# Kernel tuning notes

Hardware: AMD Instinct MI355X
Metric: run time of the kernel (lower is better)

Reference implementation:

```python
import jax, jax.numpy as jnp
import numpy as np

K, N, D, M, M_RF, N_RF = 512, 512, 16, 64, 16, 64


def cmul(a, b):
    # complex matmul with stacked real/imag in axis -3: a [...,2,m,k], b [...,2,k,n]
    ar, ai = a[..., 0, :, :], a[..., 1, :, :]
    br, bi = b[..., 0, :, :], b[..., 1, :, :]
    return jnp.stack([ar @ br - ai @ bi, ar @ bi + ai @ br], axis=-3)


def conjT(a):
    # complex conjugate transpose
    ar, ai = a[..., 0, :, :], a[..., 1, :, :]
    return jnp.stack([jnp.swapaxes(ar, -1, -2), -jnp.swapaxes(ai, -1, -2)], axis=-3)


def cinv(a):
    # inverse of complex matrix a=[2,n,n] via real 2n x 2n block matrix
    ar, ai = a[0], a[1]
    n = ar.shape[0]
    Mblk = jnp.block([[ar, -ai], [ai, ar]])
    Minv = jnp.linalg.inv(Mblk)
    return jnp.stack([Minv[:n, :n], Minv[n:, :n]], axis=0)


def setup_inputs() -> dict:
    key = jax.random.key(0)
    ks = jax.random.split(key, 8)
    s = 0.05  # keep accumulated products well-scaled
    H = s * jax.random.normal(ks[0], (K, 2, M, N), jnp.float32)
    U_RF = s * jax.random.normal(ks[1], (K, 2, M, M_RF), jnp.float32)
    U_BB = s * jax.random.normal(ks[2], (K, 2, M_RF, D), jnp.float32)
    W = s * jax.random.normal(ks[3], (K, 2, D, D), jnp.float32)
    V_RF = s * jax.random.normal(ks[4], (2, N, N_RF), jnp.float32)
    V_BB = s * jax.random.normal(ks[5], (K, 2, N_RF, D), jnp.float32)
    Y = s * jax.random.normal(ks[6], (K, 2, N, D), jnp.float32)
    rho = jnp.ones((1,), jnp.float32)  # forward arg, unused by the module
    rho_X_layer = jnp.asarray(6.0, jnp.float32)  # learned scalar
    mu = jnp.asarray(1.0, jnp.float32)           # learned scalar
    params4 = 0.001 * jax.random.normal(ks[7], (K, 2, N, D), jnp.float32)
    return dict(H=H, U_RF=U_RF, U_BB=U_BB, W=W, V_RF=V_RF, V_BB=V_BB, Y=Y,
                rho=rho, rho_X_layer=rho_X_layer, mu=mu, params4=params4)


def reference(H, U_RF, U_BB, W, V_RF, V_BB, Y, rho, rho_X_layer, mu, params4):
    # temp[k] = H[k]^H U_RF[k] U_BB[k] : [K,2,N,d]
    temp = cmul(cmul(conjT(H), U_RF), U_BB)
    TW = cmul(temp, W)  # [K,2,N,d]
    # A_rho = sum_k temp W temp^H + I/(2 rho) : [2,N,N]
    A_rho = cmul(TW, conjT(temp)).sum(axis=0)
    I = jnp.stack([jnp.eye(N, dtype=H.dtype), jnp.zeros((N, N), H.dtype)], axis=0)
    A_rho = A_rho + (1.0 / (2.0 * rho_X_layer)) * I
    # B_rho[k] = temp W + 0.5*(V_RF V_BB[k]/rho - Y[k]) : [K,2,N,d]
    B_rho = TW + 0.5 * ((1.0 / rho_X_layer) * cmul(V_RF, V_BB) - Y)
    A_inv = cinv(A_rho + mu * I)  # [2,N,N]
    X = cmul(A_inv, B_rho) + params4  # [K,2,N,d]
    return X
```

## Files before the change

### kernel.cpp

```cpp
#include <hip/hip_runtime.h>

#define KK 512
#define NN 512
#define DD 16
#define MM 64
#define MRF 16
#define NRF 64

typedef __attribute__((ext_vector_type(8))) short bf16x8;
typedef __attribute__((ext_vector_type(4))) float f32x4;
typedef __attribute__((ext_vector_type(8))) unsigned short u16x8;
typedef __attribute__((ext_vector_type(4))) unsigned short u16x4;

#define MFMA16 __builtin_amdgcn_mfma_f32_16x16x32_bf16

static __device__ __forceinline__ unsigned short f2bf(float x) {
    unsigned int u = __float_as_uint(x);
    u += 0x7fffu + ((u >> 16) & 1u);
    return (unsigned short)(u >> 16);
}
static __device__ __forceinline__ float bf2f(unsigned short b) {
    return __uint_as_float((unsigned int)b << 16);
}
static __device__ __forceinline__ unsigned int pk2(float lo, float hi) {
    return (unsigned int)f2bf(lo) | ((unsigned int)f2bf(hi) << 16);
}

union frag_cast { uint4 u; bf16x8 v; };

__global__ __launch_bounds__(256) void vrfb_kernel(
    const float* __restrict__ V_RF, unsigned short* __restrict__ VRFb)
{
    const int idx = blockIdx.x*256 + threadIdx.x;
    const int n = idx >> 7, j = idx & 127;
    const int p = j >> 6, r = j & 63;
    VRFb[idx] = f2bf(V_RF[((size_t)p*NN + n)*NRF + r]);
}

__global__ __launch_bounds__(256) void small_kernel(
    const float* __restrict__ U_RF, const float* __restrict__ U_BB,
    const float* __restrict__ W, const float* __restrict__ V_BB,
    unsigned int* __restrict__ GT2p, unsigned int* __restrict__ VBT2p)
{
    const int k = blockIdx.x, t = threadIdx.x;
    __shared__ float sUR[2][MM][17];
    __shared__ float sUB[2][MRF][DD], sW[2][DD][DD];
    __shared__ float sVB[2][NRF][17];
    __shared__ float sG[2][MM][17], sGW[2][MM][17];

    const float* uf = U_RF + (size_t)k*2*MM*MRF;
    for (int i = t; i < 2*MM*MRF; i += 256) sUR[i>>10][(i>>4)&63][i&15] = uf[i];
    const float* ub = U_BB + (size_t)k*2*MRF*DD;
    for (int i = t; i < 2*MRF*DD; i += 256) sUB[i>>8][(i>>4)&15][i&15] = ub[i];
    const float* ww = W + (size_t)k*2*DD*DD;
    for (int i = t; i < 2*DD*DD; i += 256) sW[i>>8][(i>>4)&15][i&15] = ww[i];
    const float* vb = V_BB + (size_t)k*2*NRF*DD;
    for (int i = t; i < 2*NRF*DD; i += 256) sVB[i>>10][(i>>4)&63][i&15] = vb[i];
    __syncthreads();

    {
        const int m = t >> 2, dq = (t & 3) * 4;
        float gr[4] = {0,0,0,0}, gi[4] = {0,0,0,0};
#pragma unroll
        for (int r = 0; r < MRF; ++r) {
            const float ur = sUR[0][m][r], ui = sUR[1][m][r];
#pragma unroll
            for (int q = 0; q < 4; ++q) {
                const float br = sUB[0][r][dq+q], bi = sUB[1][r][dq+q];
                gr[q] += ur*br - ui*bi;
                gi[q] += ur*bi + ui*br;
            }
        }
#pragma unroll
        for (int q = 0; q < 4; ++q) { sG[0][m][dq+q] = gr[q]; sG[1][m][dq+q] = gi[q]; }
    }
    __syncthreads();

    {
        const int m = t >> 2, dq = (t & 3) * 4;
        float gwr[4] = {0,0,0,0}, gwi[4] = {0,0,0,0};
#pragma unroll
        for (int dp = 0; dp < DD; ++dp) {
            const float gr = sG[0][m][dp], gi = sG[1][m][dp];
#pragma unroll
            for (int q = 0; q < 4; ++q) {
                const float wr = sW[0][dp][dq+q], wi = sW[1][dp][dq+q];
                gwr[q] += gr*wr - gi*wi;
                gwi[q] += gr*wi + gi*wr;
            }
        }
#pragma unroll
        for (int q = 0; q < 4; ++q) { sGW[0][m][dq+q] = gwr[q]; sGW[1][m][dq+q] = gwi[q]; }
    }
    __syncthreads();

    {
        const int e2 = t >> 2;
        const int col0 = (t & 3) * 16;
        const int m0 = (2*e2) & 63, hi0 = (2*e2) >> 6;
        const int m1 = (2*e2+1) & 63, hi1 = (2*e2+1) >> 6;
        unsigned int* dst = GT2p + ((size_t)k*64 + e2)*64 + col0;
#pragma unroll
        for (int jb = 0; jb < 4; ++jb) {
            uint4 o;
#pragma unroll
            for (int jj = 0; jj < 4; ++jj) {
                const int col = col0 + jb*4 + jj;
                const int s = col >> 4, d = col & 15;
                const float (*P)[MM][17] = (s < 2) ? sG : sGW;
                const int im = s & 1;
                float v0, v1;
                if (!im) { v0 = hi0 ? P[1][m0][d] : P[0][m0][d];
                           v1 = hi1 ? P[1][m1][d] : P[0][m1][d]; }
                else     { v0 = hi0 ? -P[0][m0][d] : P[1][m0][d];
                           v1 = hi1 ? -P[0][m1][d] : P[1][m1][d]; }
                ((unsigned int*)&o)[jj] = pk2(v0, v1);
            }
            *reinterpret_cast<uint4*>(dst + jb*4) = o;
        }
    }
    if (t < 128) {
        const int e2 = t >> 1;
        const int col0 = (t & 1) * 16;
        const int r0 = (2*e2) & 63, hi0 = (2*e2) >> 6;
        const int r1 = (2*e2+1) & 63, hi1 = (2*e2+1) >> 6;
        unsigned int* dst = VBT2p + ((size_t)k*64 + e2)*32 + col0;
#pragma unroll
        for (int jb = 0; jb < 4; ++jb) {
            uint4 o;
#pragma unroll
            for (int jj = 0; jj < 4; ++jj) {
                const int col = col0 + jb*4 + jj;
                const int s = col >> 4, d = col & 15;
                float v0, v1;
                if (s == 0) { v0 = hi0 ? -sVB[1][r0][d] : sVB[0][r0][d];
                              v1 = hi1 ? -sVB[1][r1][d] : sVB[0][r1][d]; }
                else        { v0 = hi0 ?  sVB[0][r0][d] : sVB[1][r0][d];
                              v1 = hi1 ?  sVB[0][r1][d] : sVB[1][r1][d]; }
                ((unsigned int*)&o)[jj] = pk2(v0, v1);
            }
            *reinterpret_cast<uint4*>(dst + jb*4) = o;
        }
    }
}

__global__ __launch_bounds__(512) void prep_main(
    const float* __restrict__ H, const unsigned int* __restrict__ GT2p,
    const unsigned int* __restrict__ VBT2p, const unsigned short* __restrict__ VRFb,
    const float* __restrict__ Y, const float* __restrict__ rhoX,
    unsigned short* __restrict__ tempb, unsigned short* __restrict__ TWb,
    unsigned short* __restrict__ Bb)
{
    const int nb = blockIdx.x & 3;
    const int k  = blockIdx.x >> 2;
    const int t  = threadIdx.x;
    const int n0 = nb*128;

    __shared__ unsigned int sH[64][129];
    __shared__ unsigned int sG[64][65];
    __shared__ unsigned int sV[64][33];

    const float* Hk = H + (size_t)k*128*NN + n0;
#pragma unroll
    for (int pass = 0; pass < 4; ++pass) {
        const int e2 = pass*16 + (t >> 5);
        const int c4 = (t & 31) * 4;
        const float4 a = *reinterpret_cast<const float4*>(Hk + (size_t)(2*e2  )*NN + c4);
        const float4 b = *reinterpret_cast<const float4*>(Hk + (size_t)(2*e2+1)*NN + c4);
        uint4 d;
        d.x = pk2(a.x, b.x); d.y = pk2(a.y, b.y);
        d.z = pk2(a.z, b.z); d.w = pk2(a.w, b.w);
        *reinterpret_cast<uint4*>(&sH[e2][c4]) = d;
    }
    {
        const unsigned int* g = GT2p + (size_t)k*4096;
        const int e2 = t >> 3, c0 = (t & 7) * 8;
        *reinterpret_cast<uint4*>(&sG[e2][c0])     = *reinterpret_cast<const uint4*>(g + e2*64 + c0);
        *reinterpret_cast<uint4*>(&sG[e2][c0 + 4]) = *reinterpret_cast<const uint4*>(g + e2*64 + c0 + 4);
    }
    if (t < 256) {
        const unsigned int* v = VBT2p + (size_t)k*2048;
        const int e2 = t >> 2, c0 = (t & 3) * 8;
        *reinterpret_cast<uint4*>(&sV[e2][c0])     = *reinterpret_cast<const uint4*>(v + e2*32 + c0);
        *reinterpret_cast<uint4*>(&sV[e2][c0 + 4]) = *reinterpret_cast<const uint4*>(v + e2*32 + c0 + 4);
    }
    __syncthreads();

    const int w = t >> 6, lane = t & 63;
    const int c = lane & 15, kg = lane >> 4;
    const float irx = 1.f / rhoX[0];
    const int ncol = w*16 + c;
    const int n = n0 + ncol;

    f32x4 aTr = (f32x4)0.f, aTi = (f32x4)0.f;
    f32x4 aWr = (f32x4)0.f, aWi = (f32x4)0.f;
    f32x4 aVr = (f32x4)0.f, aVi = (f32x4)0.f;

#pragma unroll
    for (int ks = 0; ks < 4; ++ks) {
        const int slot0 = ks*32 + kg*8;
        const int e2b = ks*16 + kg*4;
        frag_cast fh, g0, g1, g2, g3, v0, v1;
#pragma unroll
        for (int q = 0; q < 4; ++q) {
            ((unsigned int*)&fh.u)[q] = sH[e2b+q][ncol];
            ((unsigned int*)&g0.u)[q] = sG[e2b+q][c];
            ((unsigned int*)&g1.u)[q] = sG[e2b+q][16 + c];
            ((unsigned int*)&g2.u)[q] = sG[e2b+q][32 + c];
            ((unsigned int*)&g3.u)[q] = sG[e2b+q][48 + c];
            ((unsigned int*)&v0.u)[q] = sV[e2b+q][c];
            ((unsigned int*)&v1.u)[q] = sV[e2b+q][16 + c];
        }
        const bf16x8 bv = *reinterpret_cast<const bf16x8*>(VRFb + (size_t)n*128 + slot0);

        aTr = MFMA16(g0.v, fh.v, aTr, 0, 0, 0);
        aTi = MFMA16(g1.v, fh.v, aTi, 0, 0, 0);
        aWr = MFMA16(g2.v, fh.v, aWr, 0, 0, 0);
        aWi = MFMA16(g3.v, fh.v, aWi, 0, 0, 0);
        aVr = MFMA16(v0.v, bv, aVr, 0, 0, 0);
        aVi = MFMA16(v1.v, bv, aVi, 0, 0, 0);
    }

    {
        const size_t o0 = ((size_t)(k*2 + 0)*NN + n)*DD + kg*4;
        const size_t o1 = ((size_t)(k*2 + 1)*NN + n)*DD + kg*4;
        const float4 y0 = *reinterpret_cast<const float4*>(Y + o0);
        const float4 y1 = *reinterpret_cast<const float4*>(Y + o1);
        const float y0a[4] = {y0.x, y0.y, y0.z, y0.w};
        const float y1a[4] = {y1.x, y1.y, y1.z, y1.w};
        u16x4 tr_, ti_, wr_, wi_, br_, bi_;
#pragma unroll
        for (int r = 0; r < 4; ++r) {
            tr_[r] = f2bf(aTr[r]);  ti_[r] = f2bf(aTi[r]);
            wr_[r] = f2bf(aWr[r]);  wi_[r] = f2bf(aWi[r]);
            br_[r] = f2bf(aWr[r] + 0.5f*(aVr[r]*irx - y0a[r]));
            bi_[r] = f2bf(aWi[r] + 0.5f*(aVi[r]*irx - y1a[r]));
        }
        *reinterpret_cast<u16x4*>(tempb + o0) = tr_;
        *reinterpret_cast<u16x4*>(tempb + o1) = ti_;
        *reinterpret_cast<u16x4*>(TWb + o0)   = wr_;
        *reinterpret_cast<u16x4*>(TWb + o1)   = wi_;
        *reinterpret_cast<u16x4*>(Bb + o0)    = br_;
        *reinterpret_cast<u16x4*>(Bb + o1)    = bi_;
    }
}

__global__ __launch_bounds__(256) void egemm_kernel(
    const unsigned short* __restrict__ TWb, const unsigned short* __restrict__ tmpb,
    float* __restrict__ Epart)
{
    const int ib = blockIdx.x >> 3;
    const int ks = blockIdx.x & 7;
    const int jb = blockIdx.y;
    const int w    = threadIdx.x >> 6;
    const int lane = threadIdx.x & 63;
    const int m  = lane & 15;
    const int kg = lane >> 4;
    const int iw = ib*64 + (w>>1)*32;
    const int jw = jb*64 + (w&1)*32;
    const int d0  = (kg & 1) * 8;
    const int kof = kg >> 1;

    f32x4 RR[2][2], II[2][2], RI[2][2], IR[2][2];
#pragma unroll
    for (int is = 0; is < 2; ++is)
#pragma unroll
        for (int js = 0; js < 2; ++js) {
            RR[is][js] = (f32x4)0.f; II[is][js] = (f32x4)0.f;
            RI[is][js] = (f32x4)0.f; IR[is][js] = (f32x4)0.f;
        }

#pragma unroll 2
    for (int c = 0; c < 32; ++c) {
        const int chunk = ks*32 + c;
        const int kp = chunk*2 + kof;
        const unsigned short* Ab = TWb  + ((size_t)(kp*2+0)*NN + iw + m)*DD + d0;
        const unsigned short* Bb2 = tmpb + ((size_t)(kp*2+0)*NN + jw + m)*DD + d0;
        bf16x8 ar[2], ai[2], br[2], bi[2];
#pragma unroll
        for (int is = 0; is < 2; ++is) {
            ar[is] = *reinterpret_cast<const bf16x8*>(Ab + (size_t)is*16*DD);
            ai[is] = *reinterpret_cast<const bf16x8*>(Ab + (size_t)NN*DD + (size_t)is*16*DD);
        }
#pragma unroll
        for (int js = 0; js < 2; ++js) {
            br[js] = *reinterpret_cast<const bf16x8*>(Bb2 + (size_t)js*16*DD);
            bi[js] = *reinterpret_cast<const bf16x8*>(Bb2 + (size_t)NN*DD + (size_t)js*16*DD);
        }
#pragma unroll
        for (int is = 0; is < 2; ++is)
#pragma unroll
            for (int js = 0; js < 2; ++js) {
                RR[is][js] = MFMA16(ar[is], br[js], RR[is][js], 0, 0, 0);
                II[is][js] = MFMA16(ai[is], bi[js], II[is][js], 0, 0, 0);
                RI[is][js] = MFMA16(ar[is], bi[js], RI[is][js], 0, 0, 0);
                IR[is][js] = MFMA16(ai[is], br[js], IR[is][js], 0, 0, 0);
            }
    }

    float* Eb = Epart + (size_t)ks*2*NN*NN;
#pragma unroll
    for (int is = 0; is < 2; ++is)
#pragma unroll
        for (int js = 0; js < 2; ++js) {
            const int i = iw + is*16 + kg*4;
            const int jx = jw + js*16 + m;
#pragma unroll
            for (int r = 0; r < 4; ++r) {
                Eb[(size_t)(i+r)*NN + jx]               = RR[is][js][r] + II[is][js][r];
                Eb[(size_t)NN*NN + (size_t)(i+r)*NN + jx] = IR[is][js][r] - RI[is][js][r];
            }
        }
}

__global__ __launch_bounds__(256) void reduceinit_kernel(
    const float* __restrict__ Epart,
    const float* __restrict__ rhoX, const float* __restrict__ mu,
    unsigned short* __restrict__ P, unsigned short* __restrict__ PT,
    unsigned short* __restrict__ T1, unsigned short* __restrict__ T1T)
{
    const size_t idx = (size_t)blockIdx.x*256 + threadIdx.x;
    const float ic = 1.f / (1.f/(2.f*rhoX[0]) + mu[0]);
    const size_t pl = (size_t)2*NN*NN;
    float s = 0.f;
#pragma unroll
    for (int ks = 0; ks < 8; ++ks) s += Epart[(size_t)ks*pl + idx];
    const float mm = s * ic;
    const int p = (int)(idx / ((size_t)NN*NN));
    const size_t rem = idx - (size_t)p*NN*NN;
    const int i = (int)(rem / NN), jx = (int)(rem % NN);
    const unsigned short pv = f2bf(-mm);
    const unsigned short tv = f2bf(((p == 0 && i == jx) ? 1.f : 0.f) - mm);
    const size_t tidx = (size_t)p*NN*NN + (size_t)jx*NN + i;
    P[idx] = pv;  PT[tidx] = pv;
    T1[idx] = tv; T1T[tidx] = tv;
}

template<bool ADD_B, bool WRITE_T>
__global__ __launch_bounds__(256) void mm_kernel(
    const unsigned short* __restrict__ A, const unsigned short* __restrict__ BT,
    unsigned short* __restrict__ D, unsigned short* __restrict__ DT)
{
    const int w    = threadIdx.x >> 6;
    const int lane = threadIdx.x & 63;
    const int m  = lane & 15;
    const int kg = lane >> 4;
    const int i0 = blockIdx.y*32;
    const int j0 = blockIdx.x*32;
    const int iw = (w>>1)*16;
    const int jw = (w&1)*16;

    __shared__ unsigned short sD[2][32][34];

    f32x4 RR = (f32x4)0.f, II = (f32x4)0.f, RI = (f32x4)0.f, IR = (f32x4)0.f;

#pragma unroll 8
    for (int c = 0; c < 16; ++c) {
        const int l0 = c*32 + kg*8;
        const bf16x8 ar = *reinterpret_cast<const bf16x8*>(A  + (size_t)(i0+iw+m)*NN + l0);
        const bf16x8 ai = *reinterpret_cast<const bf16x8*>(A  + (size_t)NN*NN + (size_t)(i0+iw+m)*NN + l0);
        const bf16x8 br = *reinterpret_cast<const bf16x8*>(BT + (size_t)(j0+jw+m)*NN + l0);
        const bf16x8 bi = *reinterpret_cast<const bf16x8*>(BT + (size_t)NN*NN + (size_t)(j0+jw+m)*NN + l0);
        RR = MFMA16(ar, br, RR, 0, 0, 0);
        II = MFMA16(ai, bi, II, 0, 0, 0);
        RI = MFMA16(ar, bi, RI, 0, 0, 0);
        IR = MFMA16(ai, br, IR, 0, 0, 0);
    }
    const int i = i0 + iw + kg*4;
    const int jx = j0 + jw + m;
    float adr[4] = {0.f,0.f,0.f,0.f}, adi[4] = {0.f,0.f,0.f,0.f};
    if (ADD_B) {
        const u16x4 badr = *reinterpret_cast<const u16x4*>(BT + (size_t)jx*NN + i);
        const u16x4 badi = *reinterpret_cast<const u16x4*>(BT + (size_t)NN*NN + (size_t)jx*NN + i);
#pragma unroll
        for (int r = 0; r < 4; ++r) { adr[r] = bf2f(badr[r]); adi[r] = bf2f(badi[r]); }
    }
#pragma unroll
    for (int r = 0; r < 4; ++r) {
        const unsigned short dr_ = f2bf(RR[r] - II[r] + adr[r]);
        const unsigned short di_ = f2bf(RI[r] + IR[r] + adi[r]);
        D[(size_t)(i+r)*NN + jx] = dr_;
        D[(size_t)NN*NN + (size_t)(i+r)*NN + jx] = di_;
        if (WRITE_T) {
            sD[0][iw + kg*4 + r][jw + m] = dr_;
            sD[1][iw + kg*4 + r][jw + m] = di_;
        }
    }
    if (WRITE_T) {
        __syncthreads();
        const int t = threadIdx.x;
        const int r8 = t >> 2, seg = t & 3;
        const int plane = r8 >> 5, jloc = r8 & 31;
        u16x8 v;
#pragma unroll
        for (int e = 0; e < 8; ++e) v[e] = sD[plane][seg*8 + e][jloc];
        *reinterpret_cast<u16x8*>(DT + (size_t)plane*NN*NN +
                                  (size_t)(j0 + jloc)*NN + i0 + seg*8) = v;
    }
}

__global__ __launch_bounds__(256) void final_kernel(
    const unsigned short* __restrict__ Sb, const unsigned short* __restrict__ Bb,
    const float* __restrict__ par4,
    const float* __restrict__ rhoX, const float* __restrict__ mu,
    float* __restrict__ Xout)
{
    const int k0 = blockIdx.x * 2;
    __shared__ __align__(16) unsigned short sBT[2][2][DD][520];

#pragma unroll
    for (int kk = 0; kk < 2; ++kk) {
        const unsigned short* Bk = Bb + (size_t)(k0 + kk)*2*NN*DD;
        for (int q = 0; q < 8; ++q) {
            const int t8 = q*256 + threadIdx.x;
            const u16x8 v = *reinterpret_cast<const u16x8*>(Bk + (size_t)t8*8);
            const int flat = t8*8;
            const int p = flat >> 13, n = (flat >> 4) & 511, dd0 = flat & 15;
#pragma unroll
            for (int jj = 0; jj < 8; ++jj) sBT[kk][p][dd0+jj][n] = v[jj];
        }
    }
    __syncthreads();

    const int w    = threadIdx.x >> 6;
    const int lane = threadIdx.x & 63;
    const int m  = lane & 15;
    const int kg = lane >> 4;
    const int i0 = blockIdx.y*64 + w*16;

    f32x4 RR[2], II[2], RI[2], IR[2];
#pragma unroll
    for (int kk = 0; kk < 2; ++kk) {
        RR[kk] = (f32x4)0.f; II[kk] = (f32x4)0.f;
        RI[kk] = (f32x4)0.f; IR[kk] = (f32x4)0.f;
    }

#pragma unroll 2
    for (int c = 0; c < 16; ++c) {
        const int l0 = c*32 + kg*8;
        const bf16x8 ar = *reinterpret_cast<const bf16x8*>(Sb + (size_t)(i0+m)*NN + l0);
        const bf16x8 ai = *reinterpret_cast<const bf16x8*>(Sb + (size_t)NN*NN + (size_t)(i0+m)*NN + l0);
#pragma unroll
        for (int kk = 0; kk < 2; ++kk) {
            const bf16x8 br = *reinterpret_cast<const bf16x8*>(&sBT[kk][0][m][l0]);
            const bf16x8 bi = *reinterpret_cast<const bf16x8*>(&sBT[kk][1][m][l0]);
            RR[kk] = MFMA16(ar, br, RR[kk], 0, 0, 0);
            II[kk] = MFMA16(ai, bi, II[kk], 0, 0, 0);
            RI[kk] = MFMA16(ar, bi, RI[kk], 0, 0, 0);
            IR[kk] = MFMA16(ai, br, IR[kk], 0, 0, 0);
        }
    }
    const float ic = 1.f / (1.f/(2.f*rhoX[0]) + mu[0]);
#pragma unroll
    for (int kk = 0; kk < 2; ++kk) {
        const int k = k0 + kk;
#pragma unroll
        for (int r = 0; r < 4; ++r) {
            const int i = i0 + kg*4 + r;
            const int d = m;
            const size_t idx0 = ((size_t)(k*2+0)*NN + i)*DD + d;
            const size_t idx1 = ((size_t)(k*2+1)*NN + i)*DD + d;
            Xout[idx0] = (RR[kk][r] - II[kk][r])*ic + par4[idx0];
            Xout[idx1] = (RI[kk][r] + IR[kk][r])*ic + par4[idx1];
        }
    }
}

extern "C" void kernel_launch(void* const* d_in, const int* in_sizes, int n_in,
                              void* d_out, int out_size, void* d_ws, size_t ws_size,
                              hipStream_t stream) {
    const float* H     = (const float*)d_in[0];
    const float* U_RF  = (const float*)d_in[1];
    const float* U_BB  = (const float*)d_in[2];
    const float* W     = (const float*)d_in[3];
    const float* V_RF  = (const float*)d_in[4];
    const float* V_BB  = (const float*)d_in[5];
    const float* Y     = (const float*)d_in[6];
    const float* rhoX  = (const float*)d_in[8];
    const float* mu    = (const float*)d_in[9];
    const float* par4  = (const float*)d_in[10];
    float* Xout = (float*)d_out;

    unsigned short* u = (unsigned short*)d_ws;
    const size_t bigE = (size_t)KK*2*NN*DD;
    const size_t plE  = (size_t)2*NN*NN;
    unsigned short* tempb = u;
    unsigned short* TWb   = tempb + bigE;
    unsigned short* Bb    = TWb + bigE;
    unsigned int*   GT2p  = (unsigned int*)(Bb + bigE);
    unsigned int*   VBT2p = GT2p + (size_t)KK*4096;
    unsigned short* VRFb  = (unsigned short*)(VBT2p + (size_t)KK*2048);
    unsigned short* Pm    = VRFb + (size_t)NN*128;
    unsigned short* PmT   = Pm  + plE;
    unsigned short* T1    = PmT + plE;
    unsigned short* T1T   = T1  + plE;
    unsigned short* Q     = T1T + plE;
    unsigned short* QT    = Q   + plE;
    unsigned short* R     = QT  + plE;
    unsigned short* RT    = R   + plE;
    unsigned short* T2    = RT  + plE;
    unsigned short* T2T   = T2  + plE;
    unsigned short* T3    = T2T + plE;
    unsigned short* T3T   = T3  + plE;
    unsigned short* R2    = T3T + plE;
    unsigned short* Ss    = R2  + plE;
    float* Epart = (float*)(Ss + plE);

    vrfb_kernel<<<256, 256, 0, stream>>>(V_RF, VRFb);
    small_kernel<<<KK, 256, 0, stream>>>(U_RF, U_BB, W, V_BB, GT2p, VBT2p);
    prep_main<<<KK*4, 512, 0, stream>>>(H, GT2p, VBT2p, VRFb, Y, rhoX,
                                        tempb, TWb, Bb);
    egemm_kernel<<<dim3(64, 8), 256, 0, stream>>>(TWb, tempb, Epart);
    reduceinit_kernel<<<(int)(plE/256), 256, 0, stream>>>(Epart, rhoX, mu,
                                                          Pm, PmT, T1, T1T);
    mm_kernel<false,true ><<<dim3(16,16), 256, 0, stream>>>(Pm, PmT, Q,  QT);
    mm_kernel<true ,true ><<<dim3(16,16), 256, 0, stream>>>(Q,  T1T, T2, T2T);
    mm_kernel<false,true ><<<dim3(16,16), 256, 0, stream>>>(Q,  QT,  R,  RT);
    mm_kernel<true ,true ><<<dim3(16,16), 256, 0, stream>>>(R,  T2T, T3, T3T);
    mm_kernel<false,false><<<dim3(16,16), 256, 0, stream>>>(R,  RT,  R2, nullptr);
    mm_kernel<true ,false><<<dim3(16,16), 256, 0, stream>>>(R2, T3T, Ss, nullptr);
    final_kernel<<<dim3(KK/2, 8), 256, 0, stream>>>(Ss, Bb, par4, rhoX, mu, Xout);
}
```

Measured before the change: 216.3 us.

## Pre-swizzle G/V fragments into MFMA order and transpose H tile in LDS

small_kernel now writes the G, GW and V_BB bf16 operands in a per-lane fragment-ready layout, merged into one buffer. prep_main can then load each MFMA operand with a single 16-byte LDS read instead of many scalar reads. H is stored transposed in shared memory so its fragment is also one vector read, and the Y loads are issued before the barrier to overlap with the staging. The risk is bank conflicts from the scalar transposed stores into sHf, plus higher LDS usage per block.

Result: slower. 226.8 us (+4.8%).

```diff
diff --git a/kernel.cpp b/kernel.cpp
--- a/kernel.cpp
+++ b/kernel.cpp
@@ -40,7 +40,7 @@
 __global__ __launch_bounds__(256) void small_kernel(
     const float* __restrict__ U_RF, const float* __restrict__ U_BB,
     const float* __restrict__ W, const float* __restrict__ V_BB,
-    unsigned int* __restrict__ GT2p, unsigned int* __restrict__ VBT2p)
+    unsigned int* __restrict__ GT2f)
 {
     const int k = blockIdx.x, t = threadIdx.x;
     __shared__ float sUR[2][MM][17];
@@ -95,58 +95,42 @@
     __syncthreads();
 
     {
-        const int e2 = t >> 2;
-        const int col0 = (t & 3) * 16;
-        const int m0 = (2*e2) & 63, hi0 = (2*e2) >> 6;
-        const int m1 = (2*e2+1) & 63, hi1 = (2*e2+1) >> 6;
-        unsigned int* dst = GT2p + ((size_t)k*64 + e2)*64 + col0;
-#pragma unroll
-        for (int jb = 0; jb < 4; ++jb) {
+        const int lane64 = t & 63, ks = t >> 6;
+        const int c = lane64 & 15, kg = lane64 >> 4;
+        const int e2b = ks*16 + kg*4;
+        unsigned int* dst = GT2f + (size_t)k*6144 + lane64*96 + ks*24;
+#pragma unroll
+        for (int s = 0; s < 6; ++s) {
             uint4 o;
 #pragma unroll
-            for (int jj = 0; jj < 4; ++jj) {
-                const int col = col0 + jb*4 + jj;
-                const int s = col >> 4, d = col & 15;
-                const float (*P)[MM][17] = (s < 2) ? sG : sGW;
-                const int im = s & 1;
+            for (int j = 0; j < 4; ++j) {
+                const int e2 = e2b + j;
+                const int sl0 = 2*e2;
+                const int m0 = sl0 & 63, hi = sl0 >> 6;
+                const int m1 = m0 + 1;
                 float v0, v1;
-                if (!im) { v0 = hi0 ? P[1][m0][d] : P[0][m0][d];
-                           v1 = hi1 ? P[1][m1][d] : P[0][m1][d]; }
-                else     { v0 = hi0 ? -P[0][m0][d] : P[1][m0][d];
-                           v1 = hi1 ? -P[0][m1][d] : P[1][m1][d]; }
-                ((unsigned int*)&o)[jj] = pk2(v0, v1);
+                if (s == 0)      { v0 = hi ? sG[1][m0][c]   : sG[0][m0][c];
+                                   v1 = hi ? sG[1][m1][c]   : sG[0][m1][c]; }
+                else if (s == 1) { v0 = hi ? -sG[0][m0][c]  : sG[1][m0][c];
+                                   v1 = hi ? -sG[0][m1][c]  : sG[1][m1][c]; }
+                else if (s == 2) { v0 = hi ? sGW[1][m0][c]  : sGW[0][m0][c];
+                                   v1 = hi ? sGW[1][m1][c]  : sGW[0][m1][c]; }
+                else if (s == 3) { v0 = hi ? -sGW[0][m0][c] : sGW[1][m0][c];
+                                   v1 = hi ? -sGW[0][m1][c] : sGW[1][m1][c]; }
+                else if (s == 4) { v0 = hi ? -sVB[1][m0][c] : sVB[0][m0][c];
+                                   v1 = hi ? -sVB[1][m1][c] : sVB[0][m1][c]; }
+                else             { v0 = hi ? sVB[0][m0][c]  : sVB[1][m0][c];
+                                   v1 = hi ? sVB[0][m1][c]  : sVB[1][m1][c]; }
+                ((unsigned int*)&o)[j] = pk2(v0, v1);
             }
-            *reinterpret_cast<uint4*>(dst + jb*4) = o;
-        }
-    }
-    if (t < 128) {
-        const int e2 = t >> 1;
-        const int col0 = (t & 1) * 16;
-        const int r0 = (2*e2) & 63, hi0 = (2*e2) >> 6;
-        const int r1 = (2*e2+1) & 63, hi1 = (2*e2+1) >> 6;
-        unsigned int* dst = VBT2p + ((size_t)k*64 + e2)*32 + col0;
-#pragma unroll
-        for (int jb = 0; jb < 4; ++jb) {
-            uint4 o;
-#pragma unroll
-            for (int jj = 0; jj < 4; ++jj) {
-                const int col = col0 + jb*4 + jj;
-                const int s = col >> 4, d = col & 15;
-                float v0, v1;
-                if (s == 0) { v0 = hi0 ? -sVB[1][r0][d] : sVB[0][r0][d];
-                              v1 = hi1 ? -sVB[1][r1][d] : sVB[0][r1][d]; }
-                else        { v0 = hi0 ?  sVB[0][r0][d] : sVB[1][r0][d];
-                              v1 = hi1 ?  sVB[0][r1][d] : sVB[1][r1][d]; }
-                ((unsigned int*)&o)[jj] = pk2(v0, v1);
-            }
-            *reinterpret_cast<uint4*>(dst + jb*4) = o;
+            *reinterpret_cast<uint4*>(dst + s*4) = o;
         }
     }
 }
 
 __global__ __launch_bounds__(512) void prep_main(
-    const float* __restrict__ H, const unsigned int* __restrict__ GT2p,
-    const unsigned int* __restrict__ VBT2p, const unsigned short* __restrict__ VRFb,
+    const float* __restrict__ H, const unsigned int* __restrict__ GT2f,
+    const unsigned short* __restrict__ VRFb,
     const float* __restrict__ Y, const float* __restrict__ rhoX,
     unsigned short* __restrict__ tempb, unsigned short* __restrict__ TWb,
     unsigned short* __restrict__ Bb)
@@ -156,10 +140,16 @@
     const int t  = threadIdx.x;
     const int n0 = nb*128;
 
-    __shared__ unsigned int sH[64][129];
-    __shared__ unsigned int sG[64][65];
-    __shared__ unsigned int sV[64][33];
-
+    __shared__ unsigned int sHf[128][65];
+    __shared__ unsigned int sGf[64*97];
+
+    {
+        const unsigned int* g = GT2f + (size_t)k*6144 + t*12;
+        unsigned int* d = sGf + (t>>3)*97 + 12*(t&7);
+        *reinterpret_cast<uint4*>(d)     = *reinterpret_cast<const uint4*>(g);
+        *reinterpret_cast<uint4*>(d + 4) = *reinterpret_cast<const uint4*>(g + 4);
+        *reinterpret_cast<uint4*>(d + 8) = *reinterpret_cast<const uint4*>(g + 8);
+    }
     const float* Hk = H + (size_t)k*128*NN + n0;
 #pragma unroll
     for (int pass = 0; pass < 4; ++pass) {
@@ -167,24 +157,11 @@
         const int c4 = (t & 31) * 4;
         const float4 a = *reinterpret_cast<const float4*>(Hk + (size_t)(2*e2  )*NN + c4);
         const float4 b = *reinterpret_cast<const float4*>(Hk + (size_t)(2*e2+1)*NN + c4);
-        uint4 d;
-        d.x = pk2(a.x, b.x); d.y = pk2(a.y, b.y);
-        d.z = pk2(a.z, b.z); d.w = pk2(a.w, b.w);
-        *reinterpret_cast<uint4*>(&sH[e2][c4]) = d;
-    }
-    {
-        const unsigned int* g = GT2p + (size_t)k*4096;
-        const int e2 = t >> 3, c0 = (t & 7) * 8;
-        *reinterpret_cast<uint4*>(&sG[e2][c0])     = *reinterpret_cast<const uint4*>(g + e2*64 + c0);
-        *reinterpret_cast<uint4*>(&sG[e2][c0 + 4]) = *reinterpret_cast<const uint4*>(g + e2*64 + c0 + 4);
-    }
-    if (t < 256) {
-        const unsigned int* v = VBT2p + (size_t)k*2048;
-        const int e2 = t >> 2, c0 = (t & 3) * 8;
-        *reinterpret_cast<uint4*>(&sV[e2][c0])     = *reinterpret_cast<const uint4*>(v + e2*32 + c0);
-        *reinterpret_cast<uint4*>(&sV[e2][c0 + 4]) = *reinterpret_cast<const uint4*>(v + e2*32 + c0 + 4);
-    }
-    __syncthreads();
+        sHf[c4+0][e2] = pk2(a.x, b.x);
+        sHf[c4+1][e2] = pk2(a.y, b.y);
+        sHf[c4+2][e2] = pk2(a.z, b.z);
+        sHf[c4+3][e2] = pk2(a.w, b.w);
+    }
 
     const int w = t >> 6, lane = t & 63;
     const int c = lane & 15, kg = lane >> 4;
@@ -192,6 +169,13 @@
     const int ncol = w*16 + c;
     const int n = n0 + ncol;
 
+    const size_t o0 = ((size_t)(k*2 + 0)*NN + n)*DD + kg*4;
+    const size_t o1 = ((size_t)(k*2 + 1)*NN + n)*DD + kg*4;
+    const float4 y0 = *reinterpret_cast<const float4*>(Y + o0);
+    const float4 y1 = *reinterpret_cast<const float4*>(Y + o1);
+
+    __syncthreads();
+
     f32x4 aTr = (f32x4)0.f, aTi = (f32x4)0.f;
     f32x4 aWr = (f32x4)0.f, aWi = (f32x4)0.f;
     f32x4 aVr = (f32x4)0.f, aVi = (f32x4)0.f;
@@ -199,18 +183,15 @@
 #pragma unroll
     for (int ks = 0; ks < 4; ++ks) {
         const int slot0 = ks*32 + kg*8;
-        const int e2b = ks*16 + kg*4;
         frag_cast fh, g0, g1, g2, g3, v0, v1;
-#pragma unroll
-        for (int q = 0; q < 4; ++q) {
-            ((unsigned int*)&fh.u)[q] = sH[e2b+q][ncol];
-            ((unsigned int*)&g0.u)[q] = sG[e2b+q][c];
-            ((unsigned int*)&g1.u)[q] = sG[e2b+q][16 + c];
-            ((unsigned int*)&g2.u)[q] = sG[e2b+q][32 + c];
-            ((unsigned int*)&g3.u)[q] = sG[e2b+q][48 + c];
-            ((unsigned int*)&v0.u)[q] = sV[e2b+q][c];
-            ((unsigned int*)&v1.u)[q] = sV[e2b+q][16 + c];
-        }
+        fh.u = *reinterpret_cast<const uint4*>(&sHf[ncol][ks*16 + kg*4]);
+        const unsigned int* gb = sGf + lane*97 + ks*24;
+        g0.u = *reinterpret_cast<const uint4*>(gb);
+        g1.u = *reinterpret_cast<const uint4*>(gb + 4);
+        g2.u = *reinterpret_cast<const uint4*>(gb + 8);
+        g3.u = *reinterpret_cast<const uint4*>(gb + 12);
+        v0.u = *reinterpret_cast<const uint4*>(gb + 16);
+        v1.u = *reinterpret_cast<const uint4*>(gb + 20);
         const bf16x8 bv = *reinterpret_cast<const bf16x8*>(VRFb + (size_t)n*128 + slot0);
 
         aTr = MFMA16(g0.v, fh.v, aTr, 0, 0, 0);
@@ -222,10 +203,6 @@
     }
 
     {
-        const size_t o0 = ((size_t)(k*2 + 0)*NN + n)*DD + kg*4;
-        const size_t o1 = ((size_t)(k*2 + 1)*NN + n)*DD + kg*4;
-        const float4 y0 = *reinterpret_cast<const float4*>(Y + o0);
-        const float4 y1 = *reinterpret_cast<const float4*>(Y + o1);
         const float y0a[4] = {y0.x, y0.y, y0.z, y0.w};
         const float y1a[4] = {y1.x, y1.y, y1.z, y1.w};
         u16x4 tr_, ti_, wr_, wi_, br_, bi_;
@@ -487,9 +464,8 @@
     unsigned short* tempb = u;
     unsigned short* TWb   = tempb + bigE;
     unsigned short* Bb    = TWb + bigE;
-    unsigned int*   GT2p  = (unsigned int*)(Bb + bigE);
-    unsigned int*   VBT2p = GT2p + (size_t)KK*4096;
-    unsigned short* VRFb  = (unsigned short*)(VBT2p + (size_t)KK*2048);
+    unsigned int*   GT2f  = (unsigned int*)(Bb + bigE);
+    unsigned short* VRFb  = (unsigned short*)(GT2f + (size_t)KK*6144);
     unsigned short* Pm    = VRFb + (size_t)NN*128;
     unsigned short* PmT   = Pm  + plE;
     unsigned short* T1    = PmT + plE;
@@ -507,8 +483,8 @@
     float* Epart = (float*)(Ss + plE);
 
     vrfb_kernel<<<256, 256, 0, stream>>>(V_RF, VRFb);
-    small_kernel<<<KK, 256, 0, stream>>>(U_RF, U_BB, W, V_BB, GT2p, VBT2p);
-    prep_main<<<KK*4, 512, 0, stream>>>(H, GT2p, VBT2p, VRFb, Y, rhoX,
+    small_kernel<<<KK, 256, 0, stream>>>(U_RF, U_BB, W, V_BB, GT2f);
+    prep_main<<<KK*4, 512, 0, stream>>>(H, GT2f, VRFb, Y, rhoX,
                                         tempb, TWb, Bb);
     egemm_kernel<<<dim3(64, 8), 256, 0, stream>>>(TWb, tempb, Epart);
     reduceinit_kernel<<<(int)(plE/256), 256, 0, stream>>>(Epart, rhoX, mu,
```
